# Optimization experiments

Hardware: AMD Instinct MI355X
Metric: run time of the kernel (lower is better)

The kernel has to match this reference:

```python
import jax, jax.numpy as jnp
import numpy as np

N_EMBD = 512
N_HEAD = 8
HEAD_DIM = N_EMBD // N_HEAD
MAX_REL = 5
B, T = 8, 1024  # T must be <= 2*N_EMBD due to scores[:, :, :T, :T] slice


def setup_inputs() -> dict:
    key = jax.random.key(0)
    ks = jax.random.split(key, 10)
    C, d = N_EMBD, HEAD_DIM
    s = 1.0 / np.sqrt(C)
    return {
        "x": jax.random.normal(ks[0], (B, T, C), jnp.float32),
        # nn.Linear weights are [out, in]
        "w1_w": jax.random.normal(ks[1], (C, C), jnp.float32) * s,
        "w1_b": jnp.zeros((C,), jnp.float32),
        "w2": jax.random.uniform(ks[2], (d, 2 * C), jnp.float32, -0.001, 0.001),
        "b2": jnp.zeros((2 * C,), jnp.float32),
        "v_w": jax.random.normal(ks[3], (C, C), jnp.float32) * s,
        "v_b": jnp.zeros((C,), jnp.float32),
        "proj_w": jax.random.normal(ks[4], (C, C), jnp.float32) * s,
        "proj_b": jnp.zeros((C,), jnp.float32),
        # RelativePosition embeddings table: [2*max_rel+1, head_dim]
        "rel_v_table": jax.random.normal(ks[5], (2 * MAX_REL + 1, d), jnp.float32) * s,
    }


def reference(x, w1_w, w1_b, w2, b2, v_w, v_b, proj_w, proj_b, rel_v_table):
    Bq, Tq, C = x.shape
    H, d = N_HEAD, C // N_HEAD
    # per-position MLP synthesizer scores: relu(w1(x)) [B,H,T,d] @ w2 [d,2C] + b2
    relu_out = jax.nn.relu(x @ w1_w.T + w1_b).reshape(Bq, Tq, H, d).transpose(0, 2, 1, 3)
    scores = (relu_out @ w2 + b2)[:, :, :, :Tq]  # [B,H,T,T]
    causal = jnp.tril(jnp.ones((Tq, Tq), dtype=bool))
    scores = jnp.where(causal[None, None], scores, jnp.float32(-1e10))
    prob_attn = jax.nn.softmax(scores, axis=-1)
    # standard value path
    v = (x @ v_w.T + v_b).reshape(Bq, Tq, H, d).transpose(0, 2, 1, 3)  # [B,H,T,d]
    y1 = prob_attn @ v  # [B,H,T,d]
    # relative-position value path: table lookup per (q,k) pair
    dist = jnp.arange(Tq)[None, :] - jnp.arange(Tq)[:, None]
    idx = jnp.clip(dist, -MAX_REL, 0) + MAX_REL  # [T,T] in [0, 2*MAX_REL]
    v2 = rel_v_table[idx]  # [T,T,d]
    y2 = jnp.einsum('bhqk,qkd->bhqd', prob_attn, v2)
    y = (y1 + y2).transpose(0, 2, 1, 3).reshape(Bq, Tq, C)
    return y @ proj_w.T + proj_b
```

## Files before the change

### kernel.cpp

```cpp
#include <hip/hip_runtime.h>
#include <cstdint>

#define B_ 8
#define T_ 1024
#define C_ 512
#define H_ 8

typedef __attribute__((ext_vector_type(8))) short bf16x8;
typedef __attribute__((ext_vector_type(4))) float f32x4;

__device__ __forceinline__ unsigned short f2bf(float f) {
  uint32_t u = __float_as_uint(f);
  u += 0x7FFFu + ((u >> 16) & 1u);
  return (unsigned short)(u >> 16);
}
__device__ __forceinline__ float bf2f(unsigned short h) {
  return __uint_as_float(((uint32_t)h) << 16);
}

__device__ __forceinline__ void gload16(const void* g, void* lds) {
  __builtin_amdgcn_global_load_lds(
      (const __attribute__((address_space(1))) void*)g,
      (__attribute__((address_space(3))) void*)lds, 16, 0, 0);
}

__global__ __launch_bounds__(256) void cvt_bf16(
    const float* __restrict__ in, unsigned short* __restrict__ out, int n4) {
  int i = blockIdx.x * 256 + threadIdx.x;
  if (i < n4) {
    float4 f = reinterpret_cast<const float4*>(in)[i];
    uint2 o;
    o.x = (uint32_t)f2bf(f.x) | ((uint32_t)f2bf(f.y) << 16);
    o.y = (uint32_t)f2bf(f.z) | ((uint32_t)f2bf(f.w) << 16);
    reinterpret_cast<uint2*>(out)[i] = o;
  }
}

__global__ __launch_bounds__(256) void cvt_w3(
    const float* __restrict__ w1, const float* __restrict__ vw,
    const float* __restrict__ pw, unsigned short* __restrict__ w1b,
    unsigned short* __restrict__ vwb, unsigned short* __restrict__ pjb) {
  int seg = blockIdx.x >> 8;
  int i = (blockIdx.x & 255) * 256 + threadIdx.x;
  const float* in = (seg == 0) ? w1 : (seg == 1) ? vw : pw;
  unsigned short* o = (seg == 0) ? w1b : (seg == 1) ? vwb : pjb;
  float4 f = reinterpret_cast<const float4*>(in)[i];
  uint2 u;
  u.x = (uint32_t)f2bf(f.x) | ((uint32_t)f2bf(f.y) << 16);
  u.y = (uint32_t)f2bf(f.z) | ((uint32_t)f2bf(f.w) << 16);
  reinterpret_cast<uint2*>(o)[i] = u;
}

__global__ __launch_bounds__(256) void transpose_cvt(
    const float* __restrict__ in, unsigned short* __restrict__ out, int R, int Cc) {
  __shared__ float tile[32][33];
  const int c0 = blockIdx.x * 32, r0 = blockIdx.y * 32;
  const int t = threadIdx.x;
  {
    int ri = t >> 3, ci = (t & 7) * 4;
    float4 f = *reinterpret_cast<const float4*>(&in[(size_t)(r0 + ri) * Cc + c0 + ci]);
    tile[ri][ci] = f.x; tile[ri][ci + 1] = f.y; tile[ri][ci + 2] = f.z; tile[ri][ci + 3] = f.w;
  }
  __syncthreads();
  {
    int co = t >> 3, ro = (t & 7) * 4;
    uint2 o;
    o.x = (uint32_t)f2bf(tile[ro][co])     | ((uint32_t)f2bf(tile[ro + 1][co]) << 16);
    o.y = (uint32_t)f2bf(tile[ro + 2][co]) | ((uint32_t)f2bf(tile[ro + 3][co]) << 16);
    *reinterpret_cast<uint2*>(&out[(size_t)(c0 + co) * R + r0 + ro]) = o;
  }
}

__global__ __launch_bounds__(256) void gemm_w1v(
    const unsigned short* __restrict__ xb,
    const unsigned short* __restrict__ w1b, const unsigned short* __restrict__ vwb,
    const float* __restrict__ w1_bias, const float* __restrict__ v_bias,
    unsigned short* __restrict__ rb, unsigned short* __restrict__ vT)
{
  __shared__ alignas(16) unsigned short Xs[64 * 64];
  __shared__ alignas(16) unsigned short W1s[128 * 64];
  __shared__ alignas(16) unsigned short Vs[128 * 64];

  const int tid = threadIdx.x;
  const int lane = tid & 63, w = tid >> 6;
  const int l15 = lane & 15, g4 = lane >> 4;
  const int wr = w >> 1, wc = w & 1;
  const int n0 = blockIdx.x * 128;
  const int m0 = blockIdx.y * 64;
  const int lrow = lane >> 3;
  const int lcol = (lane & 7) * 8;

  f32x4 a1[2][4] = {};
  f32x4 a2[2][4] = {};

  for (int k0 = 0; k0 < 512; k0 += 64) {
    __syncthreads();
    #pragma unroll
    for (int cc = 0; cc < 10; ++cc) {
      int c = w * 10 + cc;
      if (c < 8) {
        gload16(&xb[(size_t)(m0 + c * 8 + lrow) * 512 + k0 + lcol],
                (char*)Xs + c * 1024);
      } else if (c < 24) {
        int cl = c - 8;
        gload16(&w1b[(size_t)(n0 + cl * 8 + lrow) * 512 + k0 + lcol],
                (char*)W1s + cl * 1024);
      } else {
        int cl = c - 24;
        gload16(&vwb[(size_t)(n0 + cl * 8 + lrow) * 512 + k0 + lcol],
                (char*)Vs + cl * 1024);
      }
    }
    __syncthreads();

    #pragma unroll
    for (int ks = 0; ks < 2; ++ks) {
      bf16x8 af[2], wf[4], vf[4];
      #pragma unroll
      for (int i = 0; i < 2; ++i)
        af[i] = *(const bf16x8*)((const char*)Xs +
                 (wr * 32 + 16 * i + l15) * 128 + ks * 64 + g4 * 16);
      #pragma unroll
      for (int j = 0; j < 4; ++j) {
        int n = wc * 64 + 16 * j + l15;
        wf[j] = *(const bf16x8*)((const char*)W1s + n * 128 + ks * 64 + g4 * 16);
        vf[j] = *(const bf16x8*)((const char*)Vs  + n * 128 + ks * 64 + g4 * 16);
      }
      #pragma unroll
      for (int i = 0; i < 2; ++i)
        #pragma unroll
        for (int j = 0; j < 4; ++j) {
          a1[i][j] = __builtin_amdgcn_mfma_f32_16x16x32_bf16(af[i], wf[j], a1[i][j], 0, 0, 0);
          a2[i][j] = __builtin_amdgcn_mfma_f32_16x16x32_bf16(af[i], vf[j], a2[i][j], 0, 0, 0);
        }
    }
  }

  #pragma unroll
  for (int i = 0; i < 2; ++i) {
    int mb = m0 + wr * 32 + 16 * i + g4 * 4;
    #pragma unroll
    for (int j = 0; j < 4; ++j) {
      int n = n0 + wc * 64 + 16 * j + l15;
      float b1 = w1_bias[n];
      #pragma unroll
      for (int rg = 0; rg < 4; ++rg)
        rb[(size_t)(mb + rg) * 512 + n] = f2bf(fmaxf(a1[i][j][rg] + b1, 0.f));
      float bv = v_bias[n];
      unsigned short p[4];
      #pragma unroll
      for (int rg = 0; rg < 4; ++rg) p[rg] = f2bf(a2[i][j][rg] + bv);
      *reinterpret_cast<uint2*>(&vT[(size_t)n * 8192 + mb]) =
          *reinterpret_cast<const uint2*>(p);
    }
  }
}

__global__ __launch_bounds__(256) void gemm_proj(
    const unsigned short* __restrict__ A, const unsigned short* __restrict__ Wb,
    const float* __restrict__ bias, float* __restrict__ out)
{
  __shared__ alignas(16) unsigned short As[64 * 64];
  __shared__ alignas(16) unsigned short Ws[128 * 64];

  const int tid = threadIdx.x;
  const int lane = tid & 63, w = tid >> 6;
  const int l15 = lane & 15, g4 = lane >> 4;
  const int wr = w >> 1, wc = w & 1;
  const int n0 = blockIdx.x * 128;
  const int m0 = blockIdx.y * 64;
  const int lrow = lane >> 3, lcol = (lane & 7) * 8;

  f32x4 acc[2][4] = {};

  for (int k0 = 0; k0 < 512; k0 += 64) {
    __syncthreads();
    #pragma unroll
    for (int cc = 0; cc < 6; ++cc) {
      int c = w * 6 + cc;
      if (c < 8) {
        gload16(&A[(size_t)(m0 + c * 8 + lrow) * 512 + k0 + lcol],
                (char*)As + c * 1024);
      } else {
        int cl = c - 8;
        gload16(&Wb[(size_t)(n0 + cl * 8 + lrow) * 512 + k0 + lcol],
                (char*)Ws + cl * 1024);
      }
    }
    __syncthreads();

    #pragma unroll
    for (int ks = 0; ks < 2; ++ks) {
      bf16x8 af[2], wf[4];
      #pragma unroll
      for (int i = 0; i < 2; ++i)
        af[i] = *(const bf16x8*)((const char*)As +
                 (wr * 32 + 16 * i + l15) * 128 + ks * 64 + g4 * 16);
      #pragma unroll
      for (int j = 0; j < 4; ++j)
        wf[j] = *(const bf16x8*)((const char*)Ws +
                 (wc * 64 + 16 * j + l15) * 128 + ks * 64 + g4 * 16);
      #pragma unroll
      for (int i = 0; i < 2; ++i)
        #pragma unroll
        for (int j = 0; j < 4; ++j)
          acc[i][j] = __builtin_amdgcn_mfma_f32_16x16x32_bf16(af[i], wf[j], acc[i][j], 0, 0, 0);
    }
  }

  #pragma unroll
  for (int i = 0; i < 2; ++i) {
    int mb = m0 + wr * 32 + 16 * i + g4 * 4;
    #pragma unroll
    for (int j = 0; j < 4; ++j) {
      int n = n0 + wc * 64 + 16 * j + l15;
      float bj = bias[n];
      #pragma unroll
      for (int rg = 0; rg < 4; ++rg)
        out[(size_t)(mb + rg) * 512 + n] = acc[i][j][rg] + bj;
    }
  }
}

#define SA_VLOAD(K0)                                                                  \
  do {                                                                                \
    { int c = tid;       int row = c >> 3, sl = c & 7;                                \
      w0 = *reinterpret_cast<const uint4*>(&w2t[(size_t)((K0) + row) * 64 + sl * 8]); } \
    { int c = tid + 256; int row = c >> 3, sl = c & 7;                                \
      w1 = *reinterpret_cast<const uint4*>(&w2t[(size_t)((K0) + row) * 64 + sl * 8]); } \
    { int c = tid;       int row = c >> 3, sl = c & 7;                                \
      v0 = *reinterpret_cast<const uint4*>(&vT[(size_t)(h * 64 + row) * 8192 + b * 1024 + (K0) + sl * 8]); } \
    { int c = tid + 256; int row = c >> 3, sl = c & 7;                                \
      v1 = *reinterpret_cast<const uint4*>(&vT[(size_t)(h * 64 + row) * 8192 + b * 1024 + (K0) + sl * 8]); } \
    if (tid < 16) bq = *reinterpret_cast<const float4*>(&b2[(K0) + tid * 4]);         \
  } while (0)

#define SA_VSTORE()                                                                   \
  do {                                                                                \
    { int c = tid;       int row = c >> 3, sl = c & 7;                                \
      *reinterpret_cast<uint4*>(W2 + row * 128 + ((sl ^ (row & 7)) << 4)) = w0; }     \
    { int c = tid + 256; int row = c >> 3, sl = c & 7;                                \
      *reinterpret_cast<uint4*>(W2 + row * 128 + ((sl ^ (row & 7)) << 4)) = w1; }     \
    { int c = tid;       int row = c >> 3, sl = c & 7;                                \
      *reinterpret_cast<uint4*>(Vt + row * 128 + ((sl ^ (row & 7)) << 4)) = v0; }     \
    { int c = tid + 256; int row = c >> 3, sl = c & 7;                                \
      *reinterpret_cast<uint4*>(Vt + row * 128 + ((sl ^ (row & 7)) << 4)) = v1; }     \
    if (tid < 16) *reinterpret_cast<float4*>(&b2L[tid * 4]) = bq;                     \
  } while (0)

__global__ __launch_bounds__(256) void synth_attn_mfma(
    const unsigned short* __restrict__ rb, const unsigned short* __restrict__ vT,
    const unsigned short* __restrict__ w2t, const float* __restrict__ b2,
    const float* __restrict__ table, unsigned short* __restrict__ ya)
{
  __shared__ alignas(16) unsigned short RtS[64 * 64];
  __shared__ alignas(16) unsigned short W2S[64 * 64];
  __shared__ alignas(16) unsigned short ElS[64 * 64];
  __shared__ alignas(16) unsigned short VtS[80 * 64];
  __shared__ float b2L[64];
  __shared__ float tap[64][5];
  __shared__ float tabs[6][64];

  char* Rt = (char*)RtS;
  char* W2 = (char*)W2S;
  char* El = (char*)ElS;
  char* Vt = (char*)VtS;

  const int tid = threadIdx.x;
  const int lane = tid & 63, w = tid >> 6;
  const int l15 = lane & 15, g = lane >> 4;
  const int bid = blockIdx.x;
  const int pp = bid & 7;
  const int bh = bid >> 3;
  const int b = bh >> 3, h = bh & 7;

  #pragma unroll
  for (int t2 = 0; t2 < 2; ++t2) {
    int idx = tid + t2 * 256;
    if (idx < 384) ((float*)tabs)[idx] = table[idx];
  }
  {
    int row = 64 + (tid >> 4), chunk = tid & 15;
    uint2 val;
    val.x = (row == 64) ? 0x3F803F80u : 0u;
    val.y = val.x;
    *reinterpret_cast<uint2*>(Vt + row * 128 + chunk * 8) = val;
  }

  uint4 w0, w1, v0, v1; float4 bq;

  for (int half = 0; half < 2; ++half) {
    const int qt = half ? (15 - pp) : pp;
    const int q0 = qt * 64;

    __syncthreads();
    #pragma unroll
    for (int t2 = 0; t2 < 2; ++t2) {
      int c = tid + t2 * 256; int row = c >> 3, sl = c & 7;
      uint4 d = *reinterpret_cast<const uint4*>(
          &rb[(size_t)(b * 1024 + q0 + row) * 512 + h * 64 + sl * 8]);
      *reinterpret_cast<uint4*>(Rt + row * 128 + ((sl ^ (row & 7)) << 4)) = d;
    }
    if (lane < 16) {
      int qr = w * 16 + lane;
      #pragma unroll
      for (int jj = 0; jj < 5; ++jj) tap[qr][jj] = 0.f;
    }

    f32x4 acc[4] = {};
    f32x4 accS = {};

    SA_VLOAD(0);
    for (int kt = 0; kt <= qt; ++kt) {
      const int k0 = kt * 64;
      __syncthreads();
      SA_VSTORE();
      if (kt < qt) SA_VLOAD(k0 + 64);
      __syncthreads();

      const int arow = w * 16 + l15;
      const int arx = l15 & 7;
      bf16x8 a0 = *reinterpret_cast<const bf16x8*>(Rt + arow * 128 + ((g ^ arx) << 4));
      bf16x8 a1 = *reinterpret_cast<const bf16x8*>(Rt + arow * 128 + (((4 + g) ^ arx) << 4));
      f32x4 sf[4] = {};
      #pragma unroll
      for (int j = 0; j < 4; ++j) {
        int row = 16 * j + l15, rx = row & 7;
        bf16x8 b0 = *reinterpret_cast<const bf16x8*>(W2 + row * 128 + ((g ^ rx) << 4));
        bf16x8 b1 = *reinterpret_cast<const bf16x8*>(W2 + row * 128 + (((4 + g) ^ rx) << 4));
        sf[j] = __builtin_amdgcn_mfma_f32_16x16x32_bf16(a0, b0, sf[j], 0, 0, 0);
        sf[j] = __builtin_amdgcn_mfma_f32_16x16x32_bf16(a1, b1, sf[j], 0, 0, 0);
      }

      if (kt == qt) {
        #pragma unroll
        for (int j = 0; j < 4; ++j) {
          int kc = 16 * j + l15;
          float bk = b2L[kc];
          #pragma unroll
          for (int rr = 0; rr < 4; ++rr) {
            int qr = w * 16 + g * 4 + rr;
            float ex = (kc <= qr) ? __expf(sf[j][rr] + bk) : 0.f;
            int byte = qr * 128 + ((((kc >> 3) ^ (qr & 7)) << 4) | ((kc & 7) << 1));
            *reinterpret_cast<unsigned short*>(El + byte) = f2bf(ex);
          }
        }
      } else {
        #pragma unroll
        for (int j = 0; j < 4; ++j) {
          int kc = 16 * j + l15;
          float bk = b2L[kc];
          #pragma unroll
          for (int rr = 0; rr < 4; ++rr) {
            int qr = w * 16 + g * 4 + rr;
            float ex = __expf(sf[j][rr] + bk);
            int byte = qr * 128 + ((((kc >> 3) ^ (qr & 7)) << 4) | ((kc & 7) << 1));
            *reinterpret_cast<unsigned short*>(El + byte) = f2bf(ex);
          }
        }
      }

      bf16x8 ae0 = *reinterpret_cast<const bf16x8*>(El + arow * 128 + ((g ^ arx) << 4));
      bf16x8 ae1 = *reinterpret_cast<const bf16x8*>(El + arow * 128 + (((4 + g) ^ arx) << 4));
      #pragma unroll
      for (int j = 0; j < 4; ++j) {
        int row = 16 * j + l15, rx = row & 7;
        bf16x8 vb0 = *reinterpret_cast<const bf16x8*>(Vt + row * 128 + ((g ^ rx) << 4));
        bf16x8 vb1 = *reinterpret_cast<const bf16x8*>(Vt + row * 128 + (((4 + g) ^ rx) << 4));
        acc[j] = __builtin_amdgcn_mfma_f32_16x16x32_bf16(ae0, vb0, acc[j], 0, 0, 0);
        acc[j] = __builtin_amdgcn_mfma_f32_16x16x32_bf16(ae1, vb1, acc[j], 0, 0, 0);
      }
      {
        int row = 64 + l15, rx = row & 7;
        bf16x8 o0 = *reinterpret_cast<const bf16x8*>(Vt + row * 128 + ((g ^ rx) << 4));
        bf16x8 o1 = *reinterpret_cast<const bf16x8*>(Vt + row * 128 + (((4 + g) ^ rx) << 4));
        accS = __builtin_amdgcn_mfma_f32_16x16x32_bf16(ae0, o0, accS, 0, 0, 0);
        accS = __builtin_amdgcn_mfma_f32_16x16x32_bf16(ae1, o1, accS, 0, 0, 0);
      }

      if (lane < 16) {
        int qr = w * 16 + lane;
        int off = q0 + qr - 4 - k0;
        #pragma unroll
        for (int jj = 0; jj < 5; ++jj) {
          int kk = off + jj;
          if ((unsigned)kk < 64u) {
            int byte = qr * 128 + ((((kk >> 3) ^ (qr & 7)) << 4) | ((kk & 7) << 1));
            tap[qr][jj] += bf2f(*reinterpret_cast<unsigned short*>(El + byte));
          }
        }
      }
    }

    float inv[4], tp[4][5];
    #pragma unroll
    for (int rr = 0; rr < 4; ++rr) {
      float ls = __shfl(accS[rr], lane & 48, 64);
      inv[rr] = 1.f / ls;
      int qr = w * 16 + g * 4 + rr;
      #pragma unroll
      for (int jj = 0; jj < 5; ++jj) tp[rr][jj] = tap[qr][jj] * inv[rr];
    }
    #pragma unroll
    for (int j = 0; j < 4; ++j) {
      int dd = 16 * j + l15;
      float t0 = tabs[0][dd];
      float dt[5];
      #pragma unroll
      for (int jj = 0; jj < 5; ++jj) dt[jj] = tabs[jj + 1][dd] - t0;
      #pragma unroll
      for (int rr = 0; rr < 4; ++rr) {
        int qr = w * 16 + g * 4 + rr;
        float y = acc[j][rr] * inv[rr] + t0;
        #pragma unroll
        for (int jj = 0; jj < 5; ++jj) y = fmaf(tp[rr][jj], dt[jj], y);
        ya[(size_t)(b * 1024 + q0 + qr) * 512 + h * 64 + dd] = f2bf(y);
      }
    }
  }
}

extern "C" void kernel_launch(void* const* d_in, const int* in_sizes, int n_in,
                              void* d_out, int out_size, void* d_ws, size_t ws_size,
                              hipStream_t stream) {
  const float* x      = (const float*)d_in[0];
  const float* w1_w   = (const float*)d_in[1];
  const float* w1_b   = (const float*)d_in[2];
  const float* w2     = (const float*)d_in[3];
  const float* b2     = (const float*)d_in[4];
  const float* v_w    = (const float*)d_in[5];
  const float* v_b    = (const float*)d_in[6];
  const float* proj_w = (const float*)d_in[7];
  const float* proj_b = (const float*)d_in[8];
  const float* relv   = (const float*)d_in[9];
  float* out = (float*)d_out;

  const size_t buf = (size_t)B_ * T_ * C_;
  const size_t wsz = (size_t)C_ * C_;
  unsigned short* rb    = (unsigned short*)d_ws;
  unsigned short* vT    = rb + buf;
  unsigned short* xb    = vT + buf;
  unsigned short* yab   = xb + buf;
  unsigned short* w1b   = yab + buf;
  unsigned short* vwb   = w1b + wsz;
  unsigned short* projb = vwb + wsz;
  unsigned short* w2t   = projb + wsz;

  cvt_bf16<<<(int)(buf / 4 + 255) / 256, 256, 0, stream>>>(x, xb, (int)(buf / 4));
  cvt_w3<<<768, 256, 0, stream>>>(w1_w, v_w, proj_w, w1b, vwb, projb);
  transpose_cvt<<<dim3(32, 2), 256, 0, stream>>>(w2, w2t, 64, 1024);

  gemm_w1v<<<dim3(4, 128), 256, 0, stream>>>(xb, w1b, vwb, w1_b, v_b, rb, vT);

  synth_attn_mfma<<<512, 256, 0, stream>>>(rb, vT, w2t, b2, relv, yab);

  gemm_proj<<<dim3(4, 128), 256, 0, stream>>>(yab, projb, proj_b, out);
}
```

Baseline: 150.7 us.

## Double-buffer GEMM and attention tiles, fuse prep kernels, vectorize score stores

Merges the three conversion/transpose prep kernels into one launch. Adds LDS double buffering to the w1/v GEMM, the projection GEMM and the synth attention loop, removing one barrier per k-step and overlapping global loads with MFMA. In attention, swaps MFMA operand order so each lane holds four consecutive keys, allowing packed 8-byte stores of exponentials, and reads b2 directly from global memory. Extra LDS usage may lower occupancy.

```diff
diff --git a/kernel.cpp b/kernel.cpp
--- a/kernel.cpp
+++ b/kernel.cpp
@@ -24,50 +24,62 @@
       (__attribute__((address_space(3))) void*)lds, 16, 0, 0);
 }
 
-__global__ __launch_bounds__(256) void cvt_bf16(
-    const float* __restrict__ in, unsigned short* __restrict__ out, int n4) {
-  int i = blockIdx.x * 256 + threadIdx.x;
-  if (i < n4) {
-    float4 f = reinterpret_cast<const float4*>(in)[i];
+__global__ __launch_bounds__(256) void prep_all(
+    const float* __restrict__ x, const float* __restrict__ w1,
+    const float* __restrict__ vw, const float* __restrict__ pw,
+    const float* __restrict__ w2,
+    unsigned short* __restrict__ xb, unsigned short* __restrict__ w1b,
+    unsigned short* __restrict__ vwb, unsigned short* __restrict__ pjb,
+    unsigned short* __restrict__ w2t)
+{
+  __shared__ float tile[32][33];
+  const int bb = blockIdx.x, t = threadIdx.x;
+  if (bb < 4096) {
+    int i = bb * 256 + t;
+    float4 f = reinterpret_cast<const float4*>(x)[i];
     uint2 o;
     o.x = (uint32_t)f2bf(f.x) | ((uint32_t)f2bf(f.y) << 16);
     o.y = (uint32_t)f2bf(f.z) | ((uint32_t)f2bf(f.w) << 16);
-    reinterpret_cast<uint2*>(out)[i] = o;
-  }
-}
-
-__global__ __launch_bounds__(256) void cvt_w3(
-    const float* __restrict__ w1, const float* __restrict__ vw,
-    const float* __restrict__ pw, unsigned short* __restrict__ w1b,
-    unsigned short* __restrict__ vwb, unsigned short* __restrict__ pjb) {
-  int seg = blockIdx.x >> 8;
-  int i = (blockIdx.x & 255) * 256 + threadIdx.x;
-  const float* in = (seg == 0) ? w1 : (seg == 1) ? vw : pw;
-  unsigned short* o = (seg == 0) ? w1b : (seg == 1) ? vwb : pjb;
-  float4 f = reinterpret_cast<const float4*>(in)[i];
-  uint2 u;
-  u.x = (uint32_t)f2bf(f.x) | ((uint32_t)f2bf(f.y) << 16);
-  u.y = (uint32_t)f2bf(f.z) | ((uint32_t)f2bf(f.w) << 16);
-  reinterpret_cast<uint2*>(o)[i] = u;
-}
-
-__global__ __launch_bounds__(256) void transpose_cvt(
-    const float* __restrict__ in, unsigned short* __restrict__ out, int R, int Cc) {
-  __shared__ float tile[32][33];
-  const int c0 = blockIdx.x * 32, r0 = blockIdx.y * 32;
-  const int t = threadIdx.x;
-  {
+    reinterpret_cast<uint2*>(xb)[i] = o;
+  } else if (bb < 4864) {
+    int seg = (bb - 4096) >> 8;
+    int i = ((bb - 4096) & 255) * 256 + t;
+    const float* in = (seg == 0) ? w1 : (seg == 1) ? vw : pw;
+    unsigned short* o = (seg == 0) ? w1b : (seg == 1) ? vwb : pjb;
+    float4 f = reinterpret_cast<const float4*>(in)[i];
+    uint2 u;
+    u.x = (uint32_t)f2bf(f.x) | ((uint32_t)f2bf(f.y) << 16);
+    u.y = (uint32_t)f2bf(f.z) | ((uint32_t)f2bf(f.w) << 16);
+    reinterpret_cast<uint2*>(o)[i] = u;
+  } else {
+    int tt = bb - 4864;
+    int c0 = (tt & 31) * 32, r0 = (tt >> 5) * 32;
     int ri = t >> 3, ci = (t & 7) * 4;
-    float4 f = *reinterpret_cast<const float4*>(&in[(size_t)(r0 + ri) * Cc + c0 + ci]);
-    tile[ri][ci] = f.x; tile[ri][ci + 1] = f.y; tile[ri][ci + 2] = f.z; tile[ri][ci + 3] = f.w;
-  }
-  __syncthreads();
-  {
+    float4 f = *reinterpret_cast<const float4*>(&w2[(size_t)(r0 + ri) * 1024 + c0 + ci]);
+    tile[ri][ci] = f.x; tile[ri][ci + 1] = f.y;
+    tile[ri][ci + 2] = f.z; tile[ri][ci + 3] = f.w;
+    __syncthreads();
     int co = t >> 3, ro = (t & 7) * 4;
     uint2 o;
     o.x = (uint32_t)f2bf(tile[ro][co])     | ((uint32_t)f2bf(tile[ro + 1][co]) << 16);
     o.y = (uint32_t)f2bf(tile[ro + 2][co]) | ((uint32_t)f2bf(tile[ro + 3][co]) << 16);
-    *reinterpret_cast<uint2*>(&out[(size_t)(c0 + co) * R + r0 + ro]) = o;
+    *reinterpret_cast<uint2*>(&w2t[(size_t)(c0 + co) * 64 + r0 + ro]) = o;
+  }
+}
+
+__device__ __forceinline__ void stg_w1v(
+    const unsigned short* xb, const unsigned short* w1b, const unsigned short* vwb,
+    char* X, char* W1, char* V, int m0, int n0, int k0, int w, int lrow, int lcol)
+{
+  #pragma unroll
+  for (int cc = 0; cc < 10; ++cc) {
+    int c = w * 10 + cc;
+    if (c < 8)
+      gload16(&xb[(size_t)(m0 + c * 8 + lrow) * 512 + k0 + lcol], X + c * 1024);
+    else if (c < 24)
+      gload16(&w1b[(size_t)(n0 + (c - 8) * 8 + lrow) * 512 + k0 + lcol], W1 + (c - 8) * 1024);
+    else
+      gload16(&vwb[(size_t)(n0 + (c - 24) * 8 + lrow) * 512 + k0 + lcol], V + (c - 24) * 1024);
   }
 }
 
@@ -77,91 +89,9 @@
     const float* __restrict__ w1_bias, const float* __restrict__ v_bias,
     unsigned short* __restrict__ rb, unsigned short* __restrict__ vT)
 {
-  __shared__ alignas(16) unsigned short Xs[64 * 64];
-  __shared__ alignas(16) unsigned short W1s[128 * 64];
-  __shared__ alignas(16) unsigned short Vs[128 * 64];
-
-  const int tid = threadIdx.x;
-  const int lane = tid & 63, w = tid >> 6;
-  const int l15 = lane & 15, g4 = lane >> 4;
-  const int wr = w >> 1, wc = w & 1;
-  const int n0 = blockIdx.x * 128;
-  const int m0 = blockIdx.y * 64;
-  const int lrow = lane >> 3;
-  const int lcol = (lane & 7) * 8;
-
-  f32x4 a1[2][4] = {};
-  f32x4 a2[2][4] = {};
-
-  for (int k0 = 0; k0 < 512; k0 += 64) {
-    __syncthreads();
-    #pragma unroll
-    for (int cc = 0; cc < 10; ++cc) {
-      int c = w * 10 + cc;
-      if (c < 8) {
-        gload16(&xb[(size_t)(m0 + c * 8 + lrow) * 512 + k0 + lcol],
-                (char*)Xs + c * 1024);
-      } else if (c < 24) {
-        int cl = c - 8;
-        gload16(&w1b[(size_t)(n0 + cl * 8 + lrow) * 512 + k0 + lcol],
-                (char*)W1s + cl * 1024);
-      } else {
-        int cl = c - 24;
-        gload16(&vwb[(size_t)(n0 + cl * 8 + lrow) * 512 + k0 + lcol],
-                (char*)Vs + cl * 1024);
-      }
-    }
-    __syncthreads();
-
-    #pragma unroll
-    for (int ks = 0; ks < 2; ++ks) {
-      bf16x8 af[2], wf[4], vf[4];
-      #pragma unroll
-      for (int i = 0; i < 2; ++i)
-        af[i] = *(const bf16x8*)((const char*)Xs +
-                 (wr * 32 + 16 * i + l15) * 128 + ks * 64 + g4 * 16);
-      #pragma unroll
-      for (int j = 0; j < 4; ++j) {
-        int n = wc * 64 + 16 * j + l15;
-        wf[j] = *(const bf16x8*)((const char*)W1s + n * 128 + ks * 64 + g4 * 16);
-        vf[j] = *(const bf16x8*)((const char*)Vs  + n * 128 + ks * 64 + g4 * 16);
-      }
-      #pragma unroll
-      for (int i = 0; i < 2; ++i)
-        #pragma unroll
-        for (int j = 0; j < 4; ++j) {
-          a1[i][j] = __builtin_amdgcn_mfma_f32_16x16x32_bf16(af[i], wf[j], a1[i][j], 0, 0, 0);
-          a2[i][j] = __builtin_amdgcn_mfma_f32_16x16x32_bf16(af[i], vf[j], a2[i][j], 0, 0, 0);
-        }
-    }
-  }
-
-  #pragma unroll
-  for (int i = 0; i < 2; ++i) {
-    int mb = m0 + wr * 32 + 16 * i + g4 * 4;
-    #pragma unroll
-    for (int j = 0; j < 4; ++j) {
-      int n = n0 + wc * 64 + 16 * j + l15;
-      float b1 = w1_bias[n];
-      #pragma unroll
-      for (int rg = 0; rg < 4; ++rg)
-        rb[(size_t)(mb + rg) * 512 + n] = f2bf(fmaxf(a1[i][j][rg] + b1, 0.f));
-      float bv = v_bias[n];
-      unsigned short p[4];
-      #pragma unroll
-      for (int rg = 0; rg < 4; ++rg) p[rg] = f2bf(a2[i][j][rg] + bv);
-      *reinterpret_cast<uint2*>(&vT[(size_t)n * 8192 + mb]) =
-          *reinterpret_cast<const uint2*>(p);
-    }
-  }
-}
-
-__global__ __launch_bounds__(256) void gemm_proj(
-    const unsigned short* __restrict__ A, const unsigned short* __restrict__ Wb,
-    const float* __restrict__ bias, float* __restrict__ out)
-{
-  __shared__ alignas(16) unsigned short As[64 * 64];
-  __shared__ alignas(16) unsigned short Ws[128 * 64];
+  __shared__ alignas(16) unsigned short Xs[2][64 * 64];
+  __shared__ alignas(16) unsigned short W1s[2][128 * 64];
+  __shared__ alignas(16) unsigned short Vs[2][128 * 64];
 
   const int tid = threadIdx.x;
   const int lane = tid & 63, w = tid >> 6;
@@ -171,35 +101,111 @@
   const int m0 = blockIdx.y * 64;
   const int lrow = lane >> 3, lcol = (lane & 7) * 8;
 
+  f32x4 a1[2][4] = {};
+  f32x4 a2[2][4] = {};
+
+  stg_w1v(xb, w1b, vwb, (char*)Xs[0], (char*)W1s[0], (char*)Vs[0],
+          m0, n0, 0, w, lrow, lcol);
+
+  for (int t = 0; t < 8; ++t) {
+    __syncthreads();
+    if (t < 7)
+      stg_w1v(xb, w1b, vwb, (char*)Xs[(t + 1) & 1], (char*)W1s[(t + 1) & 1],
+              (char*)Vs[(t + 1) & 1], m0, n0, (t + 1) * 64, w, lrow, lcol);
+    const char* Xc  = (const char*)Xs[t & 1];
+    const char* W1c = (const char*)W1s[t & 1];
+    const char* Vc  = (const char*)Vs[t & 1];
+    #pragma unroll
+    for (int ks = 0; ks < 2; ++ks) {
+      bf16x8 af[2], wf[4], vf[4];
+      #pragma unroll
+      for (int i = 0; i < 2; ++i)
+        af[i] = *(const bf16x8*)(Xc + (wr * 32 + 16 * i + l15) * 128 + ks * 64 + g4 * 16);
+      #pragma unroll
+      for (int j = 0; j < 4; ++j) {
+        int n = wc * 64 + 16 * j + l15;
+        wf[j] = *(const bf16x8*)(W1c + n * 128 + ks * 64 + g4 * 16);
+        vf[j] = *(const bf16x8*)(Vc  + n * 128 + ks * 64 + g4 * 16);
+      }
+      #pragma unroll
+      for (int i = 0; i < 2; ++i)
+        #pragma unroll
+        for (int j = 0; j < 4; ++j) {
+          a1[i][j] = __builtin_amdgcn_mfma_f32_16x16x32_bf16(af[i], wf[j], a1[i][j], 0, 0, 0);
+          a2[i][j] = __builtin_amdgcn_mfma_f32_16x16x32_bf16(af[i], vf[j], a2[i][j], 0, 0, 0);
+        }
+    }
+  }
+
+  #pragma unroll
+  for (int i = 0; i < 2; ++i) {
+    int mb = m0 + wr * 32 + 16 * i + g4 * 4;
+    #pragma unroll
+    for (int j = 0; j < 4; ++j) {
+      int n = n0 + wc * 64 + 16 * j + l15;
+      float b1 = w1_bias[n];
+      #pragma unroll
+      for (int rg = 0; rg < 4; ++rg)
+        rb[(size_t)(mb + rg) * 512 + n] = f2bf(fmaxf(a1[i][j][rg] + b1, 0.f));
+      float bv = v_bias[n];
+      unsigned short p[4];
+      #pragma unroll
+      for (int rg = 0; rg < 4; ++rg) p[rg] = f2bf(a2[i][j][rg] + bv);
+      *reinterpret_cast<uint2*>(&vT[(size_t)n * 8192 + mb]) =
+          *reinterpret_cast<const uint2*>(p);
+    }
+  }
+}
+
+__device__ __forceinline__ void stg_proj(
+    const unsigned short* A, const unsigned short* Wb,
+    char* As, char* Ws, int m0, int n0, int k0, int w, int lrow, int lcol)
+{
+  #pragma unroll
+  for (int cc = 0; cc < 6; ++cc) {
+    int c = w * 6 + cc;
+    if (c < 8)
+      gload16(&A[(size_t)(m0 + c * 8 + lrow) * 512 + k0 + lcol], As + c * 1024);
+    else
+      gload16(&Wb[(size_t)(n0 + (c - 8) * 8 + lrow) * 512 + k0 + lcol], Ws + (c - 8) * 1024);
+  }
+}
+
+__global__ __launch_bounds__(256) void gemm_proj(
+    const unsigned short* __restrict__ A, const unsigned short* __restrict__ Wb,
+    const float* __restrict__ bias, float* __restrict__ out)
+{
+  __shared__ alignas(16) unsigned short As[2][64 * 64];
+  __shared__ alignas(16) unsigned short Ws[2][128 * 64];
+
+  const int tid = threadIdx.x;
+  const int lane = tid & 63, w = tid >> 6;
+  const int l15 = lane & 15, g4 = lane >> 4;
+  const int wr = w >> 1, wc = w & 1;
+  const int n0 = blockIdx.x * 128;
+  const int m0 = blockIdx.y * 64;
+  const int lrow = lane >> 3, lcol = (lane & 7) * 8;
+
   f32x4 acc[2][4] = {};
 
-  for (int k0 = 0; k0 < 512; k0 += 64) {
+  stg_proj(A, Wb, (char*)As[0], (char*)Ws[0], m0, n0, 0, w, lrow, lcol);
+
+  for (int t = 0; t < 8; ++t) {
     __syncthreads();
-    #pragma unroll
-    for (int cc = 0; cc < 6; ++cc) {
-      int c = w * 6 + cc;
-      if (c < 8) {
-        gload16(&A[(size_t)(m0 + c * 8 + lrow) * 512 + k0 + lcol],
-                (char*)As + c * 1024);
-      } else {
-        int cl = c - 8;
-        gload16(&Wb[(size_t)(n0 + cl * 8 + lrow) * 512 + k0 + lcol],
-                (char*)Ws + cl * 1024);
-      }
-    }
-    __syncthreads();
-
+    if (t < 7)
+      stg_proj(A, Wb, (char*)As[(t + 1) & 1], (char*)Ws[(t + 1) & 1],
+               m0, n0, (t + 1) * 64, w, lrow, lcol);
+    const char* Ac = (const char*)As[t & 1];
+    const char* Wc = (const char*)Ws[t & 1];
     #pragma unroll
     for (int ks = 0; ks < 2; ++ks) {
       bf16x8 af[2], wf[4];
       #pragma unroll
       for (int i = 0; i < 2; ++i)
-        af[i] = *(const bf16x8*)((const char*)As +
-                 (wr * 32 + 16 * i + l15) * 128 + ks * 64 + g4 * 16);
+        af[i] = *(const bf16x8*)(Ac + (wr * 32 + 16 * i + l15) * 128 + ks * 64 + g4 * 16);
       #pragma unroll
       for (int j = 0; j < 4; ++j)
-        wf[j] = *(const bf16x8*)((const char*)Ws +
-                 (wc * 64 + 16 * j + l15) * 128 + ks * 64 + g4 * 16);
+        wf[j] = *(const bf16x8*)(Wc + (wc * 64 + 16 * j + l15) * 128 + ks * 64 + g4 * 16);
       #pragma unroll
       for (int i = 0; i < 2; ++i)
         #pragma unroll
@@ -232,20 +238,18 @@
       v0 = *reinterpret_cast<const uint4*>(&vT[(size_t)(h * 64 + row) * 8192 + b * 1024 + (K0) + sl * 8]); } \
     { int c = tid + 256; int row = c >> 3, sl = c & 7;                                \
       v1 = *reinterpret_cast<const uint4*>(&vT[(size_t)(h * 64 + row) * 8192 + b * 1024 + (K0) + sl * 8]); } \
-    if (tid < 16) bq = *reinterpret_cast<const float4*>(&b2[(K0) + tid * 4]);         \
   } while (0)
 
-#define SA_VSTORE()                                                                   \
+#define SA_VSTORE(W2B, VTB)                                                           \
   do {                                                                                \
     { int c = tid;       int row = c >> 3, sl = c & 7;                                \
-      *reinterpret_cast<uint4*>(W2 + row * 128 + ((sl ^ (row & 7)) << 4)) = w0; }     \
+      *reinterpret_cast<uint4*>((char*)(W2B) + row * 128 + ((sl ^ (row & 7)) << 4)) = w0; } \
     { int c = tid + 256; int row = c >> 3, sl = c & 7;                                \
-      *reinterpret_cast<uint4*>(W2 + row * 128 + ((sl ^ (row & 7)) << 4)) = w1; }     \
+      *reinterpret_cast<uint4*>((char*)(W2B) + row * 128 + ((sl ^ (row & 7)) << 4)) = w1; } \
     { int c = tid;       int row = c >> 3, sl = c & 7;                                \
-      *reinterpret_cast<uint4*>(Vt + row * 128 + ((sl ^ (row & 7)) << 4)) = v0; }     \
+      *reinterpret_cast<uint4*>((char*)(VTB) + row * 128 + ((sl ^ (row & 7)) << 4)) = v0; } \
     { int c = tid + 256; int row = c >> 3, sl = c & 7;                                \
-      *reinterpret_cast<uint4*>(Vt + row * 128 + ((sl ^ (row & 7)) << 4)) = v1; }     \
-    if (tid < 16) *reinterpret_cast<float4*>(&b2L[tid * 4]) = bq;                     \
+      *reinterpret_cast<uint4*>((char*)(VTB) + row * 128 + ((sl ^ (row & 7)) << 4)) = v1; } \
   } while (0)
 
 __global__ __launch_bounds__(256) void synth_attn_mfma(
@@ -254,17 +258,14 @@
     const float* __restrict__ table, unsigned short* __restrict__ ya)
 {
   __shared__ alignas(16) unsigned short RtS[64 * 64];
-  __shared__ alignas(16) unsigned short W2S[64 * 64];
   __shared__ alignas(16) unsigned short ElS[64 * 64];
-  __shared__ alignas(16) unsigned short VtS[80 * 64];
-  __shared__ float b2L[64];
+  __shared__ alignas(16) unsigned short W2S[2][64 * 64];
+  __shared__ alignas(16) unsigned short VtS[2][80 * 64];
   __shared__ float tap[64][5];
   __shared__ float tabs[6][64];
 
   char* Rt = (char*)RtS;
-  char* W2 = (char*)W2S;
   char* El = (char*)ElS;
-  char* Vt = (char*)VtS;
 
   const int tid = threadIdx.x;
   const int lane = tid & 63, w = tid >> 6;
@@ -273,6 +274,8 @@
   const int pp = bid & 7;
   const int bh = bid >> 3;
   const int b = bh >> 3, h = bh & 7;
+  const int qrl = 16 * w + l15;
+  const int sx = l15 & 7;
 
   #pragma unroll
   for (int t2 = 0; t2 < 2; ++t2) {
@@ -280,14 +283,15 @@
     if (idx < 384) ((float*)tabs)[idx] = table[idx];
   }
   {
-    int row = 64 + (tid >> 4), chunk = tid & 15;
+    int row = 64 + (tid >> 4), ch = tid & 15;
     uint2 val;
     val.x = (row == 64) ? 0x3F803F80u : 0u;
     val.y = val.x;
-    *reinterpret_cast<uint2*>(Vt + row * 128 + chunk * 8) = val;
-  }
-
-  uint4 w0, w1, v0, v1; float4 bq;
+    *reinterpret_cast<uint2*>((char*)VtS[0] + row * 128 + ch * 8) = val;
+    *reinterpret_cast<uint2*>((char*)VtS[1] + row * 128 + ch * 8) = val;
+  }
+
+  uint4 w0, w1, v0, v1;
 
   for (int half = 0; half < 2; ++half) {
     const int qt = half ? (15 - pp) : pp;
@@ -311,69 +315,70 @@
     f32x4 accS = {};
 
     SA_VLOAD(0);
+    SA_VSTORE(W2S[0], VtS[0]);
+
     for (int kt = 0; kt <= qt; ++kt) {
       const int k0 = kt * 64;
+      const int cur = kt & 1;
       __syncthreads();
-      SA_VSTORE();
+
+      float4 bq0 = *reinterpret_cast<const float4*>(&b2[k0 +  0 + 4 * g]);
+      float4 bq1 = *reinterpret_cast<const float4*>(&b2[k0 + 16 + 4 * g]);
+      float4 bq2 = *reinterpret_cast<const float4*>(&b2[k0 + 32 + 4 * g]);
+      float4 bq3 = *reinterpret_cast<const float4*>(&b2[k0 + 48 + 4 * g]);
       if (kt < qt) SA_VLOAD(k0 + 64);
-      __syncthreads();
-
-      const int arow = w * 16 + l15;
-      const int arx = l15 & 7;
-      bf16x8 a0 = *reinterpret_cast<const bf16x8*>(Rt + arow * 128 + ((g ^ arx) << 4));
-      bf16x8 a1 = *reinterpret_cast<const bf16x8*>(Rt + arow * 128 + (((4 + g) ^ arx) << 4));
+
+      const char* W2c = (const char*)W2S[cur];
+      const char* Vtc = (const char*)VtS[cur];
+
+      bf16x8 rb0 = *(const bf16x8*)(Rt + qrl * 128 + ((g ^ sx) << 4));
+      bf16x8 rb1 = *(const bf16x8*)(Rt + qrl * 128 + (((4 + g) ^ sx) << 4));
       f32x4 sf[4] = {};
       #pragma unroll
       for (int j = 0; j < 4; ++j) {
-        int row = 16 * j + l15, rx = row & 7;
-        bf16x8 b0 = *reinterpret_cast<const bf16x8*>(W2 + row * 128 + ((g ^ rx) << 4));
-        bf16x8 b1 = *reinterpret_cast<const bf16x8*>(W2 + row * 128 + (((4 + g) ^ rx) << 4));
-        sf[j] = __builtin_amdgcn_mfma_f32_16x16x32_bf16(a0, b0, sf[j], 0, 0, 0);
-        sf[j] = __builtin_amdgcn_mfma_f32_16x16x32_bf16(a1, b1, sf[j], 0, 0, 0);
-      }
-
-      if (kt == qt) {
-        #pragma unroll
-        for (int j = 0; j < 4; ++j) {
-          int kc = 16 * j + l15;
-          float bk = b2L[kc];
-          #pragma unroll
-          for (int rr = 0; rr < 4; ++rr) {
-            int qr = w * 16 + g * 4 + rr;
-            float ex = (kc <= qr) ? __expf(sf[j][rr] + bk) : 0.f;
-            int byte = qr * 128 + ((((kc >> 3) ^ (qr & 7)) << 4) | ((kc & 7) << 1));
-            *reinterpret_cast<unsigned short*>(El + byte) = f2bf(ex);
-          }
+        int ar = 16 * j + l15;
+        bf16x8 wa0 = *(const bf16x8*)(W2c + ar * 128 + ((g ^ sx) << 4));
+        bf16x8 wa1 = *(const bf16x8*)(W2c + ar * 128 + (((4 + g) ^ sx) << 4));
+        sf[j] = __builtin_amdgcn_mfma_f32_16x16x32_bf16(wa0, rb0, sf[j], 0, 0, 0);
+        sf[j] = __builtin_amdgcn_mfma_f32_16x16x32_bf16(wa1, rb1, sf[j], 0, 0, 0);
+      }
+
+      const bool diag = (kt == qt);
+      #pragma unroll
+      for (int j = 0; j < 4; ++j) {
+        const float4 bq = (j == 0) ? bq0 : (j == 1) ? bq1 : (j == 2) ? bq2 : bq3;
+        const int kb = 16 * j + 4 * g;
+        float e0 = __expf(sf[j][0] + bq.x);
+        float e1 = __expf(sf[j][1] + bq.y);
+        float e2 = __expf(sf[j][2] + bq.z);
+        float e3 = __expf(sf[j][3] + bq.w);
+        if (diag) {
+          e0 = (kb + 0 <= qrl) ? e0 : 0.f;
+          e1 = (kb + 1 <= qrl) ? e1 : 0.f;
+          e2 = (kb + 2 <= qrl) ? e2 : 0.f;
+          e3 = (kb + 3 <= qrl) ? e3 : 0.f;
         }
-      } else {
-        #pragma unroll
-        for (int j = 0; j < 4; ++j) {
-          int kc = 16 * j + l15;
-          float bk = b2L[kc];
-          #pragma unroll
-          for (int rr = 0; rr < 4; ++rr) {
-            int qr = w * 16 + g * 4 + rr;
-            float ex = __expf(sf[j][rr] + bk);
-            int byte = qr * 128 + ((((kc >> 3) ^ (qr & 7)) << 4) | ((kc & 7) << 1));
-            *reinterpret_cast<unsigned short*>(El + byte) = f2bf(ex);
-          }
-        }
-      }
-
-      bf16x8 ae0 = *reinterpret_cast<const bf16x8*>(El + arow * 128 + ((g ^ arx) << 4));
-      bf16x8 ae1 = *reinterpret_cast<const bf16x8*>(El + arow * 128 + (((4 + g) ^ arx) << 4));
+        uint2 pk;
+        pk.x = (uint32_t)f2bf(e0) | ((uint32_t)f2bf(e1) << 16);
+        pk.y = (uint32_t)f2bf(e2) | ((uint32_t)f2bf(e3) << 16);
+        int slot = (2 * j + (g >> 1)) ^ sx;
+        *reinterpret_cast<uint2*>(El + qrl * 128 + slot * 16 + (g & 1) * 8) = pk;
+      }
+
+      bf16x8 ae0 = *(const bf16x8*)(El + qrl * 128 + ((g ^ sx) << 4));
+      bf16x8 ae1 = *(const bf16x8*)(El + qrl * 128 + (((4 + g) ^ sx) << 4));
       #pragma unroll
       for (int j = 0; j < 4; ++j) {
-        int row = 16 * j + l15, rx = row & 7;
-        bf16x8 vb0 = *reinterpret_cast<const bf16x8*>(Vt + row * 128 + ((g ^ rx) << 4));
-        bf16x8 vb1 = *reinterpret_cast<const bf16x8*>(Vt + row * 128 + (((4 + g) ^ rx) << 4));
+        int vr = 16 * j + l15;
+        bf16x8 vb0 = *(const bf16x8*)(Vtc + vr * 128 + ((g ^ sx) << 4));
+        bf16x8 vb1 = *(const bf16x8*)(Vtc + vr * 128 + (((4 + g) ^ sx) << 4));
         acc[j] = __builtin_amdgcn_mfma_f32_16x16x32_bf16(ae0, vb0, acc[j], 0, 0, 0);
         acc[j] = __builtin_amdgcn_mfma_f32_16x16x32_bf16(ae1, vb1, acc[j], 0, 0, 0);
       }
       {
-        int row = 64 + l15, rx = row & 7;
-        bf16x8 o0 = *reinterpret_cast<const bf16x8*>(Vt + row * 128 + ((g ^ rx) << 4));
-        bf16x8 o1 = *reinterpret_cast<const bf16x8*>(Vt + row * 128 + (((4 + g) ^ rx) << 4));
+        int orow = 64 + l15;
+        bf16x8 o0 = *(const bf16x8*)(Vtc + orow * 128 + ((g ^ sx) << 4));
+        bf16x8 o1 = *(const bf16x8*)(Vtc + orow * 128 + (((4 + g) ^ sx) << 4));
         accS = __builtin_amdgcn_mfma_f32_16x16x32_bf16(ae0, o0, accS, 0, 0, 0);
         accS = __builtin_amdgcn_mfma_f32_16x16x32_bf16(ae1, o1, accS, 0, 0, 0);
       }
@@ -390,6 +395,8 @@
           }
         }
       }
+
+      if (kt < qt) SA_VSTORE(W2S[(kt + 1) & 1], VtS[(kt + 1) & 1]);
     }
 
     float inv[4], tp[4][5];
@@ -446,9 +453,8 @@
   unsigned short* projb = vwb + wsz;
   unsigned short* w2t   = projb + wsz;
 
-  cvt_bf16<<<(int)(buf / 4 + 255) / 256, 256, 0, stream>>>(x, xb, (int)(buf / 4));
-  cvt_w3<<<768, 256, 0, stream>>>(w1_w, v_w, proj_w, w1b, vwb, projb);
-  transpose_cvt<<<dim3(32, 2), 256, 0, stream>>>(w2, w2t, 64, 1024);
+  prep_all<<<4928, 256, 0, stream>>>(x, w1_w, v_w, proj_w, w2,
+                                     xb, w1b, vwb, projb, w2t);
 
   gemm_w1v<<<dim3(4, 128), 256, 0, stream>>>(xb, w1b, vwb, w1_b, v_b, rb, vT);
 
```

Result: faster. 142.5 us (-5.4%).
